# Optimization experiments

Hardware: AMD Instinct MI355X
Metric: run time of the kernel (lower is better)

## Reference

```python
import jax, jax.numpy as jnp
import numpy as np

Q = 256    # ques_size (feat_size)
H = 256    # seq_hidden_size
T = 500000 # history length
K = 32     # attn_k


def setup_inputs() -> dict:
    key = jax.random.key(0)
    ks = jax.random.split(key, 10)
    s = 0.05
    return {
        "ques_h": jax.random.normal(ks[0], (Q,), dtype=jnp.float32),
        "score": jax.random.uniform(ks[1], (1,), dtype=jnp.float32),
        "qs": jax.random.normal(ks[2], (T, Q), dtype=jnp.float32),
        "hs": jax.random.normal(ks[3], (T, H), dtype=jnp.float32),
        # GRU params (torch gate order: reset, update, new)
        "W_ih": jax.random.normal(ks[4], (3 * H, 2 * Q), dtype=jnp.float32) * s,
        "W_hh": jax.random.normal(ks[5], (3 * H, H), dtype=jnp.float32) * s,
        "b_ih": jax.random.normal(ks[6], (3 * H,), dtype=jnp.float32) * s,
        "b_hh": jax.random.normal(ks[7], (3 * H,), dtype=jnp.float32) * s,
        # score_net: Linear(Q + H, 1)
        "W_s": jax.random.normal(ks[8], (1, Q + H), dtype=jnp.float32) * s,
        "b_s": jax.random.normal(ks[9], (1,), dtype=jnp.float32) * s,
        "attn_k": K,
    }


def reference(ques_h, score, qs, hs, W_ih, W_hh, b_ih, b_hh, W_s, b_s, attn_k):
    # --- top-k attention over history ---
    alpha = qs @ ques_h                       # [T] similarity matvec
    vals, idx = jax.lax.top_k(alpha, attn_k)  # k = min(T, attn_k); T >> k
    w = jax.nn.softmax(vals)                  # [k]
    attn_h = w @ hs[idx]                      # gather [k,H] then weighted sum -> [H]

    # --- score prediction ---
    pred = W_s @ jnp.concatenate([ques_h, attn_h]) + b_s  # [1]

    # --- score-gated GRU input ---
    ge = (score >= 0.5).astype(ques_h.dtype)              # [1], broadcasts
    x = jnp.concatenate([ques_h * ge, ques_h * (1.0 - ge)])  # [2Q]

    # --- single-step GRU (torch semantics) ---
    h_prev = hs[-1]                            # [H]
    gi = W_ih @ x + b_ih                       # [3H]
    gh = W_hh @ h_prev + b_hh                  # [3H]
    i_r, i_z, i_n = jnp.split(gi, 3)
    h_r, h_z, h_n = jnp.split(gh, 3)
    r = jax.nn.sigmoid(i_r + h_r)
    z = jax.nn.sigmoid(i_z + h_z)
    n = jnp.tanh(i_n + r * h_n)
    h_new = (1.0 - z) * n + z * h_prev         # [H]

    # --- history append (torch.cat bookkeeping in SP.forward) ---
    qs_new = jnp.concatenate([qs, ques_h[None, :]], axis=0)  # [T+1, Q]
    hs_new = jnp.concatenate([hs, h_new[None, :]], axis=0)   # [T+1, H]
    return (pred, qs_new, hs_new)
```

## Files before the change

### kernel.cpp

```cpp
#include <hip/hip_runtime.h>
#include <math.h>

constexpr int kT = 500000;
constexpr int kQ = 256;
constexpr int kH = 256;
constexpr int kK = 32;
constexpr int kNB1 = 256;
constexpr int kCHUNK = (kT + kNB1 - 1) / kNB1;
constexpr int kNC = kNB1 * kK;
constexpr int kGruRows = 3 * kH;
constexpr int kGruBlocks = kGruRows / 4;
constexpr int kRowsQs = kT + 1;
constexpr int kRowsAll = 2 * kT + 2;

typedef float f4 __attribute__((ext_vector_type(4)));

constexpr size_t kScratchFloats = (size_t)kT + 2 * kNC + 2 * kGruRows + kH;

__global__ __launch_bounds__(256) void k_bigcopy(
    const float* __restrict__ qs, const float* __restrict__ hs,
    const float* __restrict__ qh, const float* __restrict__ hnew,
    float* __restrict__ out, float* __restrict__ alpha,
    int rowBegin, int rowEnd) {
  const int lane = threadIdx.x & 63;
  const int wid  = (int)((blockIdx.x * blockDim.x + threadIdx.x) >> 6);
  const int nw   = (int)((gridDim.x * blockDim.x) >> 6);
  const f4 q4 = ((const f4*)qh)[lane];
  for (int r = rowBegin + wid; r < rowEnd; r += nw) {
    const f4* src;
    if (r < kT)               src = (const f4*)(qs + (size_t)r * kQ);
    else if (r == kT)         src = (const f4*)qh;
    else if (r < 2 * kT + 1)  src = (const f4*)(hs + (size_t)(r - kT - 1) * kH);
    else                      src = (const f4*)hnew;
    f4 v = src[lane];
    float pw = __shfl_up(v.w, 1);
    float* obase = out + 1 + (size_t)r * kQ;
    if (lane > 0) {
      f4 sv; sv.x = pw; sv.y = v.x; sv.z = v.y; sv.w = v.z;
      *(f4*)(obase - 1 + 4 * lane) = sv;
    } else {
      obase[0] = v.x; obase[1] = v.y; obase[2] = v.z;
    }
    if (lane == 63) obase[255] = v.w;
    if (r < kT) {
      float d = v.x * q4.x + v.y * q4.y + v.z * q4.z + v.w * q4.w;
#pragma unroll
      for (int off = 32; off; off >>= 1) d += __shfl_xor(d, off);
      if (lane == 0) alpha[r] = d;
    }
  }
}

__global__ __launch_bounds__(256) void k_gru1(
    const float* __restrict__ Wih, const float* __restrict__ Whh,
    const float* __restrict__ bih, const float* __restrict__ bhh,
    const float* __restrict__ qh, const float* __restrict__ hs,
    const float* __restrict__ score, float* __restrict__ gi,
    float* __restrict__ gh) {
  const int lane = threadIdx.x & 63;
  const int r = blockIdx.x * 4 + (threadIdx.x >> 6);
  const int off = (score[0] >= 0.5f) ? 0 : kQ;
  const float* hprev = hs + (size_t)(kT - 1) * kH;
  f4 q4 = ((const f4*)qh)[lane];
  f4 h4 = ((const f4*)hprev)[lane];
  f4 wi = ((const f4*)(Wih + (size_t)r * (2 * kQ) + off))[lane];
  f4 wh = ((const f4*)(Whh + (size_t)r * kH))[lane];
  float di = wi.x * q4.x + wi.y * q4.y + wi.z * q4.z + wi.w * q4.w;
  float dh = wh.x * h4.x + wh.y * h4.y + wh.z * h4.z + wh.w * h4.w;
#pragma unroll
  for (int o = 32; o; o >>= 1) {
    di += __shfl_xor(di, o);
    dh += __shfl_xor(dh, o);
  }
  if (lane == 0) {
    gi[r] = di + bih[r];
    gh[r] = dh + bhh[r];
  }
}

__global__ __launch_bounds__(256) void k_gru2(
    const float* __restrict__ gi, const float* __restrict__ gh,
    const float* __restrict__ hs, float* __restrict__ hnew_dst) {
  const int i = threadIdx.x;
  const float* hprev = hs + (size_t)(kT - 1) * kH;
  float rr = 1.f / (1.f + expf(-(gi[i] + gh[i])));
  float z  = 1.f / (1.f + expf(-(gi[kH + i] + gh[kH + i])));
  float n  = tanhf(gi[2 * kH + i] + rr * gh[2 * kH + i]);
  hnew_dst[i] = (1.f - z) * n + z * hprev[i];
}

__global__ __launch_bounds__(256) void k_topk1(
    const float* __restrict__ alpha, float* __restrict__ candV,
    int* __restrict__ candI) {
  __shared__ float sv[kCHUNK];
  __shared__ float rv[4];
  __shared__ int ri[4];
  const int tid = threadIdx.x;
  const int base = blockIdx.x * kCHUNK;
  for (int i = tid; i < kCHUNK; i += 256) {
    int g = base + i;
    sv[i] = (g < kT) ? alpha[g] : -INFINITY;
  }
  __syncthreads();
  for (int k = 0; k < kK; ++k) {
    float bv = -INFINITY; int bi = -1;
    for (int i = tid; i < kCHUNK; i += 256) {
      float v = sv[i];
      if (v > bv) { bv = v; bi = i; }
    }
#pragma unroll
    for (int off = 32; off; off >>= 1) {
      float ov = __shfl_xor(bv, off);
      int   oi = __shfl_xor(bi, off);
      if (ov > bv || (ov == bv && oi != -1 && (bi == -1 || oi < bi))) { bv = ov; bi = oi; }
    }
    if ((tid & 63) == 0) { rv[tid >> 6] = bv; ri[tid >> 6] = bi; }
    __syncthreads();
    if (tid == 0) {
      float fv = rv[0]; int fi = ri[0];
      for (int j = 1; j < 4; ++j)
        if (rv[j] > fv || (rv[j] == fv && ri[j] != -1 && (fi == -1 || ri[j] < fi))) {
          fv = rv[j]; fi = ri[j];
        }
      candV[blockIdx.x * kK + k] = fv;
      candI[blockIdx.x * kK + k] = (fi >= 0) ? (base + fi) : 0;
      if (fi >= 0) sv[fi] = -INFINITY;
    }
    __syncthreads();
  }
}

__global__ __launch_bounds__(256) void k_attn(
    const float* __restrict__ candV, const int* __restrict__ candI,
    const float* __restrict__ hs, const float* __restrict__ qh,
    const float* __restrict__ Ws, const float* __restrict__ bs,
    float* __restrict__ out) {
  __shared__ float sv[kNC];
  __shared__ float rv[4];
  __shared__ int ri[4];
  __shared__ float topv[kK];
  __shared__ int topi[kK];
  __shared__ float w[kK];
  __shared__ float red[256];
  const int tid = threadIdx.x;
  for (int i = tid; i < kNC; i += 256) sv[i] = candV[i];
  __syncthreads();
  for (int k = 0; k < kK; ++k) {
    float bv = -INFINITY; int bi = -1;
    for (int i = tid; i < kNC; i += 256) {
      float v = sv[i];
      if (v > bv) { bv = v; bi = i; }
    }
#pragma unroll
    for (int off = 32; off; off >>= 1) {
      float ov = __shfl_xor(bv, off);
      int   oi = __shfl_xor(bi, off);
      if (ov > bv || (ov == bv && oi != -1 && (bi == -1 || oi < bi))) { bv = ov; bi = oi; }
    }
    if ((tid & 63) == 0) { rv[tid >> 6] = bv; ri[tid >> 6] = bi; }
    __syncthreads();
    if (tid == 0) {
      float fv = rv[0]; int fi = ri[0];
      for (int j = 1; j < 4; ++j)
        if (rv[j] > fv || (rv[j] == fv && ri[j] != -1 && (fi == -1 || ri[j] < fi))) {
          fv = rv[j]; fi = ri[j];
        }
      topv[k] = fv;
      topi[k] = candI[fi];
      sv[fi] = -INFINITY;
    }
    __syncthreads();
  }
  if (tid == 0) {
    float m = topv[0];
    for (int j = 1; j < kK; ++j) m = fmaxf(m, topv[j]);
    float s = 0.f;
    for (int j = 0; j < kK; ++j) { w[j] = expf(topv[j] - m); s += w[j]; }
    float inv = 1.f / s;
    for (int j = 0; j < kK; ++j) w[j] *= inv;
  }
  __syncthreads();
  float a = 0.f;
#pragma unroll
  for (int j = 0; j < kK; ++j) a += w[j] * hs[(size_t)topi[j] * kH + tid];
  red[tid] = Ws[tid] * qh[tid] + Ws[kQ + tid] * a;
  __syncthreads();
  for (int s = 128; s; s >>= 1) {
    if (tid < s) red[tid] += red[tid + s];
    __syncthreads();
  }
  if (tid == 0) out[0] = red[0] + bs[0];
}

extern "C" void kernel_launch(void* const* d_in, const int* in_sizes, int n_in,
                              void* d_out, int out_size, void* d_ws, size_t ws_size,
                              hipStream_t stream) {
  const float* qh    = (const float*)d_in[0];
  const float* score = (const float*)d_in[1];
  const float* qs    = (const float*)d_in[2];
  const float* hs    = (const float*)d_in[3];
  const float* Wih   = (const float*)d_in[4];
  const float* Whh   = (const float*)d_in[5];
  const float* bih   = (const float*)d_in[6];
  const float* bhh   = (const float*)d_in[7];
  const float* Ws    = (const float*)d_in[8];
  const float* bs    = (const float*)d_in[9];
  float* out = (float*)d_out;

  const bool useWs = ws_size >= kScratchFloats * sizeof(float);
  float* S = useWs ? (float*)d_ws : (out + 1 + (size_t)(kT + 1) * kQ);
  float* alpha = S;
  float* candV = S + kT;
  int*   candI = (int*)(S + kT + kNC);
  float* gi    = S + kT + 2 * kNC;
  float* gh    = gi + kGruRows;
  float* hnew  = gh + kGruRows;

  if (useWs) {
    hipLaunchKernelGGL(k_gru1, dim3(kGruBlocks), dim3(256), 0, stream,
                       Wih, Whh, bih, bhh, qh, hs, score, gi, gh);
    hipLaunchKernelGGL(k_gru2, dim3(1), dim3(256), 0, stream,
                       gi, gh, hs, hnew);
    hipLaunchKernelGGL(k_bigcopy, dim3(2048), dim3(256), 0, stream,
                       qs, hs, qh, hnew, out, alpha, 0, kRowsAll);
    hipLaunchKernelGGL(k_topk1, dim3(kNB1), dim3(256), 0, stream,
                       alpha, candV, candI);
    hipLaunchKernelGGL(k_attn, dim3(1), dim3(256), 0, stream,
                       candV, candI, hs, qh, Ws, bs, out);
  } else {
    float* hnewOut = out + 1 + (size_t)(kT + 1) * kQ + (size_t)kT * kH;
    hipLaunchKernelGGL(k_gru1, dim3(kGruBlocks), dim3(256), 0, stream,
                       Wih, Whh, bih, bhh, qh, hs, score, gi, gh);
    hipLaunchKernelGGL(k_gru2, dim3(1), dim3(256), 0, stream,
                       gi, gh, hs, hnewOut);
    hipLaunchKernelGGL(k_bigcopy, dim3(2048), dim3(256), 0, stream,
                       qs, hs, qh, hnewOut, out, alpha, 0, kRowsQs);
    hipLaunchKernelGGL(k_topk1, dim3(kNB1), dim3(256), 0, stream,
                       alpha, candV, candI);
    hipLaunchKernelGGL(k_attn, dim3(1), dim3(256), 0, stream,
                       candV, candI, hs, qh, Ws, bs, out);
    hipLaunchKernelGGL(k_bigcopy, dim3(2048), dim3(256), 0, stream,
                       qs, hs, qh, hnewOut, out, alpha, kRowsQs, 2 * kT + 1);
  }
}
```

Before: 604.1 us.

## Unroll copy loop 4x with unaligned vector stores and partial-sum alpha

```diff
diff --git a/kernel.cpp b/kernel.cpp
--- a/kernel.cpp
+++ b/kernel.cpp
@@ -14,39 +14,70 @@
 constexpr int kRowsAll = 2 * kT + 2;
 
 typedef float f4 __attribute__((ext_vector_type(4)));
-
-constexpr size_t kScratchFloats = (size_t)kT + 2 * kNC + 2 * kGruRows + kH;
+typedef float f4u __attribute__((ext_vector_type(4), aligned(4)));
+
+constexpr size_t kScratchFloats = 4 * (size_t)kT + 2 * kNC + 2 * kGruRows + kH;
+
+__device__ __forceinline__ const f4* row_src(
+    int r, const float* __restrict__ qs, const float* __restrict__ hs,
+    const float* __restrict__ qh, const float* __restrict__ hnew) {
+  if (r < kT)          return (const f4*)(qs + (size_t)r * kQ);
+  if (r == kT)         return (const f4*)qh;
+  if (r < 2 * kT + 1)  return (const f4*)(hs + (size_t)(r - kT - 1) * kH);
+  return (const f4*)hnew;
+}
+
+__device__ __forceinline__ float dot4(f4 a, f4 b) {
+  return a.x * b.x + a.y * b.y + a.z * b.z + a.w * b.w;
+}
 
 __global__ __launch_bounds__(256) void k_bigcopy(
     const float* __restrict__ qs, const float* __restrict__ hs,
     const float* __restrict__ qh, const float* __restrict__ hnew,
-    float* __restrict__ out, float* __restrict__ alpha,
+    float* __restrict__ out, float* __restrict__ alpha4,
     int rowBegin, int rowEnd) {
   const int lane = threadIdx.x & 63;
   const int wid  = (int)((blockIdx.x * blockDim.x + threadIdx.x) >> 6);
   const int nw   = (int)((gridDim.x * blockDim.x) >> 6);
   const f4 q4 = ((const f4*)qh)[lane];
-  for (int r = rowBegin + wid; r < rowEnd; r += nw) {
-    const f4* src;
-    if (r < kT)               src = (const f4*)(qs + (size_t)r * kQ);
-    else if (r == kT)         src = (const f4*)qh;
-    else if (r < 2 * kT + 1)  src = (const f4*)(hs + (size_t)(r - kT - 1) * kH);
-    else                      src = (const f4*)hnew;
-    f4 v = src[lane];
-    float pw = __shfl_up(v.w, 1);
-    float* obase = out + 1 + (size_t)r * kQ;
-    if (lane > 0) {
-      f4 sv; sv.x = pw; sv.y = v.x; sv.z = v.y; sv.w = v.z;
-      *(f4*)(obase - 1 + 4 * lane) = sv;
-    } else {
-      obase[0] = v.x; obase[1] = v.y; obase[2] = v.z;
-    }
-    if (lane == 63) obase[255] = v.w;
-    if (r < kT) {
-      float d = v.x * q4.x + v.y * q4.y + v.z * q4.z + v.w * q4.w;
-#pragma unroll
-      for (int off = 32; off; off >>= 1) d += __shfl_xor(d, off);
-      if (lane == 0) alpha[r] = d;
+  const int g = lane >> 4;
+  const bool wr = (lane & 15) == 0;
+
+  int t = rowBegin + wid;
+  for (; t + 3 * nw < rowEnd; t += 4 * nw) {
+    const int r0 = t, r1 = t + nw, r2 = t + 2 * nw, r3 = t + 3 * nw;
+    f4 v0 = row_src(r0, qs, hs, qh, hnew)[lane];
+    f4 v1 = row_src(r1, qs, hs, qh, hnew)[lane];
+    f4 v2 = row_src(r2, qs, hs, qh, hnew)[lane];
+    f4 v3 = row_src(r3, qs, hs, qh, hnew)[lane];
+    *(f4u*)(out + 1 + (size_t)r0 * kQ + 4 * lane) = v0;
+    *(f4u*)(out + 1 + (size_t)r1 * kQ + 4 * lane) = v1;
+    *(f4u*)(out + 1 + (size_t)r2 * kQ + 4 * lane) = v2;
+    *(f4u*)(out + 1 + (size_t)r3 * kQ + 4 * lane) = v3;
+    float d0 = dot4(v0, q4), d1 = dot4(v1, q4);
+    float d2 = dot4(v2, q4), d3 = dot4(v3, q4);
+#pragma unroll
+    for (int off = 8; off; off >>= 1) {
+      d0 += __shfl_xor(d0, off);
+      d1 += __shfl_xor(d1, off);
+      d2 += __shfl_xor(d2, off);
+      d3 += __shfl_xor(d3, off);
+    }
+    if (wr) {
+      if (r0 < kT) alpha4[4 * r0 + g] = d0;
+      if (r1 < kT) alpha4[4 * r1 + g] = d1;
+      if (r2 < kT) alpha4[4 * r2 + g] = d2;
+      if (r3 < kT) alpha4[4 * r3 + g] = d3;
+    }
+  }
+  for (; t < rowEnd; t += nw) {
+    f4 v = row_src(t, qs, hs, qh, hnew)[lane];
+    *(f4u*)(out + 1 + (size_t)t * kQ + 4 * lane) = v;
+    if (t < kT) {
+      float d = dot4(v, q4);
+#pragma unroll
+      for (int off = 8; off; off >>= 1) d += __shfl_xor(d, off);
+      if (wr) alpha4[4 * t + g] = d;
     }
   }
 }
@@ -65,8 +96,8 @@
   f4 h4 = ((const f4*)hprev)[lane];
   f4 wi = ((const f4*)(Wih + (size_t)r * (2 * kQ) + off))[lane];
   f4 wh = ((const f4*)(Whh + (size_t)r * kH))[lane];
-  float di = wi.x * q4.x + wi.y * q4.y + wi.z * q4.z + wi.w * q4.w;
-  float dh = wh.x * h4.x + wh.y * h4.y + wh.z * h4.z + wh.w * h4.w;
+  float di = dot4(wi, q4);
+  float dh = dot4(wh, h4);
 #pragma unroll
   for (int o = 32; o; o >>= 1) {
     di += __shfl_xor(di, o);
@@ -90,7 +121,7 @@
 }
 
 __global__ __launch_bounds__(256) void k_topk1(
-    const float* __restrict__ alpha, float* __restrict__ candV,
+    const float* __restrict__ alpha4, float* __restrict__ candV,
     int* __restrict__ candI) {
   __shared__ float sv[kCHUNK];
   __shared__ float rv[4];
@@ -98,8 +129,13 @@
   const int tid = threadIdx.x;
   const int base = blockIdx.x * kCHUNK;
   for (int i = tid; i < kCHUNK; i += 256) {
-    int g = base + i;
-    sv[i] = (g < kT) ? alpha[g] : -INFINITY;
+    int gidx = base + i;
+    if (gidx < kT) {
+      f4 a = ((const f4*)alpha4)[gidx];
+      sv[i] = (a.x + a.y) + (a.z + a.w);
+    } else {
+      sv[i] = -INFINITY;
+    }
   }
   __syncthreads();
   for (int k = 0; k < kK; ++k) {
@@ -209,10 +245,10 @@
 
   const bool useWs = ws_size >= kScratchFloats * sizeof(float);
   float* S = useWs ? (float*)d_ws : (out + 1 + (size_t)(kT + 1) * kQ);
-  float* alpha = S;
-  float* candV = S + kT;
-  int*   candI = (int*)(S + kT + kNC);
-  float* gi    = S + kT + 2 * kNC;
+  float* alpha4 = S;
+  float* candV = S + 4 * (size_t)kT;
+  int*   candI = (int*)(candV + kNC);
+  float* gi    = candV + 2 * kNC;
   float* gh    = gi + kGruRows;
   float* hnew  = gh + kGruRows;
 
@@ -222,9 +258,9 @@
     hipLaunchKernelGGL(k_gru2, dim3(1), dim3(256), 0, stream,
                        gi, gh, hs, hnew);
     hipLaunchKernelGGL(k_bigcopy, dim3(2048), dim3(256), 0, stream,
-                       qs, hs, qh, hnew, out, alpha, 0, kRowsAll);
+                       qs, hs, qh, hnew, out, alpha4, 0, kRowsAll);
     hipLaunchKernelGGL(k_topk1, dim3(kNB1), dim3(256), 0, stream,
-                       alpha, candV, candI);
+                       alpha4, candV, candI);
     hipLaunchKernelGGL(k_attn, dim3(1), dim3(256), 0, stream,
                        candV, candI, hs, qh, Ws, bs, out);
   } else {
@@ -234,12 +270,12 @@
     hipLaunchKernelGGL(k_gru2, dim3(1), dim3(256), 0, stream,
                        gi, gh, hs, hnewOut);
     hipLaunchKernelGGL(k_bigcopy, dim3(2048), dim3(256), 0, stream,
-                       qs, hs, qh, hnewOut, out, alpha, 0, kRowsQs);
+                       qs, hs, qh, hnewOut, out, alpha4, 0, kRowsQs);
     hipLaunchKernelGGL(k_topk1, dim3(kNB1), dim3(256), 0, stream,
-                       alpha, candV, candI);
+                       alpha4, candV, candI);
     hipLaunchKernelGGL(k_attn, dim3(1), dim3(256), 0, stream,
                        candV, candI, hs, qh, Ws, bs, out);
     hipLaunchKernelGGL(k_bigcopy, dim3(2048), dim3(256), 0, stream,
-                       qs, hs, qh, hnewOut, out, alpha, kRowsQs, 2 * kT + 1);
-  }
-}
+                       qs, hs, qh, hnewOut, out, alpha4, kRowsQs, 2 * kT + 1);
+  }
+}
```

Result: slower. 636.1 us (+5.3%).

## Split fused copy into standalone alpha kernel plus device memcpy for history

Applied to the files above, without the earlier changes.

```diff
diff --git a/kernel.cpp b/kernel.cpp
--- a/kernel.cpp
+++ b/kernel.cpp
@@ -10,44 +10,28 @@
 constexpr int kNC = kNB1 * kK;
 constexpr int kGruRows = 3 * kH;
 constexpr int kGruBlocks = kGruRows / 4;
-constexpr int kRowsQs = kT + 1;
-constexpr int kRowsAll = 2 * kT + 2;
 
 typedef float f4 __attribute__((ext_vector_type(4)));
 
-constexpr size_t kScratchFloats = (size_t)kT + 2 * kNC + 2 * kGruRows + kH;
-
-__global__ __launch_bounds__(256) void k_bigcopy(
-    const float* __restrict__ qs, const float* __restrict__ hs,
-    const float* __restrict__ qh, const float* __restrict__ hnew,
-    float* __restrict__ out, float* __restrict__ alpha,
-    int rowBegin, int rowEnd) {
+__device__ __forceinline__ float dot4(f4 a, f4 b) {
+  return a.x * b.x + a.y * b.y + a.z * b.z + a.w * b.w;
+}
+
+constexpr size_t kScratchFloats = (size_t)kT + 2 * kNC + 2 * kGruRows;
+
+__global__ __launch_bounds__(256) void k_alpha(
+    const float* __restrict__ qs, const float* __restrict__ qh,
+    float* __restrict__ alpha) {
   const int lane = threadIdx.x & 63;
   const int wid  = (int)((blockIdx.x * blockDim.x + threadIdx.x) >> 6);
   const int nw   = (int)((gridDim.x * blockDim.x) >> 6);
   const f4 q4 = ((const f4*)qh)[lane];
-  for (int r = rowBegin + wid; r < rowEnd; r += nw) {
-    const f4* src;
-    if (r < kT)               src = (const f4*)(qs + (size_t)r * kQ);
-    else if (r == kT)         src = (const f4*)qh;
-    else if (r < 2 * kT + 1)  src = (const f4*)(hs + (size_t)(r - kT - 1) * kH);
-    else                      src = (const f4*)hnew;
-    f4 v = src[lane];
-    float pw = __shfl_up(v.w, 1);
-    float* obase = out + 1 + (size_t)r * kQ;
-    if (lane > 0) {
-      f4 sv; sv.x = pw; sv.y = v.x; sv.z = v.y; sv.w = v.z;
-      *(f4*)(obase - 1 + 4 * lane) = sv;
-    } else {
-      obase[0] = v.x; obase[1] = v.y; obase[2] = v.z;
-    }
-    if (lane == 63) obase[255] = v.w;
-    if (r < kT) {
-      float d = v.x * q4.x + v.y * q4.y + v.z * q4.z + v.w * q4.w;
-#pragma unroll
-      for (int off = 32; off; off >>= 1) d += __shfl_xor(d, off);
-      if (lane == 0) alpha[r] = d;
-    }
+  for (int t = wid; t < kT; t += nw) {
+    f4 v = ((const f4*)(qs + (size_t)t * kQ))[lane];
+    float d = dot4(v, q4);
+#pragma unroll
+    for (int off = 32; off; off >>= 1) d += __shfl_xor(d, off);
+    if (lane == 0) alpha[t] = d;
   }
 }
 
@@ -65,8 +49,8 @@
   f4 h4 = ((const f4*)hprev)[lane];
   f4 wi = ((const f4*)(Wih + (size_t)r * (2 * kQ) + off))[lane];
   f4 wh = ((const f4*)(Whh + (size_t)r * kH))[lane];
-  float di = wi.x * q4.x + wi.y * q4.y + wi.z * q4.z + wi.w * q4.w;
-  float dh = wh.x * h4.x + wh.y * h4.y + wh.z * h4.z + wh.w * h4.w;
+  float di = dot4(wi, q4);
+  float dh = dot4(wh, h4);
 #pragma unroll
   for (int o = 32; o; o >>= 1) {
     di += __shfl_xor(di, o);
@@ -78,15 +62,21 @@
   }
 }
 
-__global__ __launch_bounds__(256) void k_gru2(
+__global__ __launch_bounds__(256) void k_finalrows(
     const float* __restrict__ gi, const float* __restrict__ gh,
-    const float* __restrict__ hs, float* __restrict__ hnew_dst) {
+    const float* __restrict__ hs, const float* __restrict__ qh,
+    float* __restrict__ out) {
   const int i = threadIdx.x;
+  if (blockIdx.x == 1) {
+    out[1 + (size_t)kT * kQ + i] = qh[i];
+    return;
+  }
   const float* hprev = hs + (size_t)(kT - 1) * kH;
   float rr = 1.f / (1.f + expf(-(gi[i] + gh[i])));
   float z  = 1.f / (1.f + expf(-(gi[kH + i] + gh[kH + i])));
   float n  = tanhf(gi[2 * kH + i] + rr * gh[2 * kH + i]);
-  hnew_dst[i] = (1.f - z) * n + z * hprev[i];
+  out[1 + (size_t)(kT + 1) * kQ + (size_t)kT * kH + i] =
+      (1.f - z) * n + z * hprev[i];
 }
 
 __global__ __launch_bounds__(256) void k_topk1(
@@ -211,35 +201,24 @@
   float* S = useWs ? (float*)d_ws : (out + 1 + (size_t)(kT + 1) * kQ);
   float* alpha = S;
   float* candV = S + kT;
-  int*   candI = (int*)(S + kT + kNC);
-  float* gi    = S + kT + 2 * kNC;
+  int*   candI = (int*)(candV + kNC);
+  float* gi    = candV + 2 * kNC;
   float* gh    = gi + kGruRows;
-  float* hnew  = gh + kGruRows;
-
-  if (useWs) {
-    hipLaunchKernelGGL(k_gru1, dim3(kGruBlocks), dim3(256), 0, stream,
-                       Wih, Whh, bih, bhh, qh, hs, score, gi, gh);
-    hipLaunchKernelGGL(k_gru2, dim3(1), dim3(256), 0, stream,
-                       gi, gh, hs, hnew);
-    hipLaunchKernelGGL(k_bigcopy, dim3(2048), dim3(256), 0, stream,
-                       qs, hs, qh, hnew, out, alpha, 0, kRowsAll);
-    hipLaunchKernelGGL(k_topk1, dim3(kNB1), dim3(256), 0, stream,
-                       alpha, candV, candI);
-    hipLaunchKernelGGL(k_attn, dim3(1), dim3(256), 0, stream,
-                       candV, candI, hs, qh, Ws, bs, out);
-  } else {
-    float* hnewOut = out + 1 + (size_t)(kT + 1) * kQ + (size_t)kT * kH;
-    hipLaunchKernelGGL(k_gru1, dim3(kGruBlocks), dim3(256), 0, stream,
-                       Wih, Whh, bih, bhh, qh, hs, score, gi, gh);
-    hipLaunchKernelGGL(k_gru2, dim3(1), dim3(256), 0, stream,
-                       gi, gh, hs, hnewOut);
-    hipLaunchKernelGGL(k_bigcopy, dim3(2048), dim3(256), 0, stream,
-                       qs, hs, qh, hnewOut, out, alpha, 0, kRowsQs);
-    hipLaunchKernelGGL(k_topk1, dim3(kNB1), dim3(256), 0, stream,
-                       alpha, candV, candI);
-    hipLaunchKernelGGL(k_attn, dim3(1), dim3(256), 0, stream,
-                       candV, candI, hs, qh, Ws, bs, out);
-    hipLaunchKernelGGL(k_bigcopy, dim3(2048), dim3(256), 0, stream,
-                       qs, hs, qh, hnewOut, out, alpha, kRowsQs, 2 * kT + 1);
-  }
-}
+
+  hipLaunchKernelGGL(k_gru1, dim3(kGruBlocks), dim3(256), 0, stream,
+                     Wih, Whh, bih, bhh, qh, hs, score, gi, gh);
+  hipLaunchKernelGGL(k_finalrows, dim3(2), dim3(256), 0, stream,
+                     gi, gh, hs, qh, out);
+  hipLaunchKernelGGL(k_alpha, dim3(2048), dim3(256), 0, stream,
+                     qs, qh, alpha);
+  hipLaunchKernelGGL(k_topk1, dim3(kNB1), dim3(256), 0, stream,
+                     alpha, candV, candI);
+  hipLaunchKernelGGL(k_attn, dim3(1), dim3(256), 0, stream,
+                     candV, candI, hs, qh, Ws, bs, out);
+
+  hipMemcpyAsync(out + 1, qs, (size_t)kT * kQ * sizeof(float),
+                 hipMemcpyDeviceToDevice, stream);
+  hipMemcpyAsync(out + 1 + (size_t)(kT + 1) * kQ, hs,
+                 (size_t)kT * kH * sizeof(float),
+                 hipMemcpyDeviceToDevice, stream);
+}
```

Measured after the change: 907.2 us. +50.2%, slower.
